# Performance work log

Hardware: AMD Instinct MI355X
Metric: run time of the kernel (lower is better)

Reference implementation:

```python
import jax, jax.numpy as jnp
import numpy as np

N0, K3, K2 = 262144, 27, 8
N1, N2 = N0 // 8, N0 // 64
CIN, C0, C1, C2 = 3, 24, 48, 96
EPS = 1e-5


def _conv_bn_relu(x, neigh, W, gamma, beta):
    # Octree sparse conv: gather neighbor features and contract with kernel.
    # x: [N, Cin], neigh: [M, K] int indices into N, W: [K, Cin, Cout]
    y = jnp.einsum('mkc,kcd->md', x[neigh], W)
    # BatchNorm1d (training-mode batch statistics) + ReLU
    mu = jnp.mean(y, axis=0)
    var = jnp.var(y, axis=0)
    y = (y - mu) * jax.lax.rsqrt(var + EPS) * gamma + beta
    return jax.nn.relu(y)


def setup_inputs() -> dict:
    key = jax.random.key(0)
    k = jax.random.split(key, 16)

    def w(kk, shape, fan):
        return jax.random.normal(kk, shape, jnp.float32) / np.float32(np.sqrt(fan))

    return {
        'data':   jax.random.normal(k[0], (N0, CIN), jnp.float32),
        'neigh0': jax.random.randint(k[1], (N0, K3), 0, N0, jnp.int32),
        'child0': jax.random.randint(k[2], (N1, K2), 0, N0, jnp.int32),
        'neigh1': jax.random.randint(k[3], (N1, K3), 0, N1, jnp.int32),
        'child1': jax.random.randint(k[4], (N2, K2), 0, N1, jnp.int32),
        'neigh2': jax.random.randint(k[5], (N2, K3), 0, N2, jnp.int32),
        'w0':  w(k[6],  (K3, CIN, C0), K3 * CIN),
        'g0':  jnp.ones((C0,), jnp.float32),  'b0':  jnp.zeros((C0,), jnp.float32),
        'wd0': w(k[7],  (K2, C0, C1),  K2 * C0),
        'gd0': jnp.ones((C1,), jnp.float32),  'bd0': jnp.zeros((C1,), jnp.float32),
        'w1':  w(k[8],  (K3, C1, C1),  K3 * C1),
        'g1':  jnp.ones((C1,), jnp.float32),  'b1':  jnp.zeros((C1,), jnp.float32),
        'wd1': w(k[9],  (K2, C1, C2),  K2 * C1),
        'gd1': jnp.ones((C2,), jnp.float32),  'bd1': jnp.zeros((C2,), jnp.float32),
        'wp':  w(k[10], (K3, C2, C2),  K3 * C2),
        'gp':  jnp.ones((C2,), jnp.float32),  'bp':  jnp.zeros((C2,), jnp.float32),
    }


def reference(data, neigh0, child0, neigh1, child1, neigh2,
              w0, g0, b0, wd0, gd0, bd0, w1, g1, b1, wd1, gd1, bd1, wp, gp, bp):
    # stage 0 at depth d: conv3 then stride-2 downsample
    x = _conv_bn_relu(data, neigh0, w0, g0, b0)      # [N0, 24]
    x = _conv_bn_relu(x, child0, wd0, gd0, bd0)      # [N1, 48]
    # stage 1 at depth d-1
    x = _conv_bn_relu(x, neigh1, w1, g1, b1)         # [N1, 48]
    x = _conv_bn_relu(x, child1, wd1, gd1, bd1)      # [N2, 96]
    # proj at depth d-2
    x = _conv_bn_relu(x, neigh2, wp, gp, bp)         # [N2, 96]
    return x
```

## Files before the change

kernel.cpp:

```cpp
#include <hip/hip_runtime.h>

#define N0 262144
#define N1 32768
#define N2 4096
#define EPSBN 1e-5f

typedef unsigned short ush_t;
typedef __bf16 bf16x8 __attribute__((ext_vector_type(8)));
typedef float  f32x4  __attribute__((ext_vector_type(4)));

union ufcast { unsigned int u; float f; };
__device__ __forceinline__ float bflo(unsigned int p) { ufcast x; x.u = p << 16;          return x.f; }
__device__ __forceinline__ float bfhi(unsigned int p) { ufcast x; x.u = p & 0xffff0000u; return x.f; }
__device__ __forceinline__ ush_t f2bf(float f) {
    ufcast x; x.f = f;
    unsigned int u = x.u + 0x7fffu + ((x.u >> 16) & 1u);
    return (ush_t)(u >> 16);
}
__device__ __forceinline__ bf16x8 as_bf8(uint4 u) {
    union { uint4 u; bf16x8 b; } x; x.u = u; return x.b;
}

template<int C, int NB>
__device__ __forceinline__ void compute_ss(const float* __restrict__ bins,
                                           const float* __restrict__ g, const float* __restrict__ b,
                                           float M, float* ssl)
{
    const int tid = threadIdx.x;
    if (tid < 2 * C) {
        float s = 0.f;
#pragma unroll
        for (int k = 0; k < NB; ++k) s += bins[k * 2 * C + tid];
        ssl[tid] = s;
    }
    __syncthreads();
    if (tid < C) {
        const float mu  = ssl[tid] / M;
        const float var = fmaxf(ssl[C + tid] / M - mu * mu, 0.f);
        const float sc  = g[tid] / sqrtf(var + EPSBN);
        const float sh  = b[tid] - mu * sc;
        ssl[tid] = sc; ssl[C + tid] = sh;
    }
    __syncthreads();
}

template<int K, int CIN, int CINP_W, int COUT, int COUTP, int NCH>
__device__ __forceinline__ void prep_stage(const float* __restrict__ W, ush_t* __restrict__ Wb, int e) {
    const int k  = e & 31;
    const int n  = (e >> 5) % COUTP;
    const int ch = e / (32 * COUTP);
    const int kp = ch * 32 + k;
    const int t  = kp / CINP_W;
    const int c  = kp % CINP_W;
    float v = 0.f;
    if (t < K && c < CIN && n < COUT) v = W[((size_t)t * CIN + c) * COUT + n];
    Wb[e] = f2bf(v);
}

#define BINS_TOTAL 9984

__global__ __launch_bounds__(256) void prep_all(
    const float* w0, const float* wd0, const float* w1, const float* wd1, const float* wp,
    const float* data,
    ush_t* wbA, ush_t* wbB, ush_t* wbC, ush_t* wbD, ush_t* wbE, ush_t* xa, float* binsz)
{
    const int e = blockIdx.x * 256 + threadIdx.x;
    switch (blockIdx.y) {
        case 0: if (e <   4096) prep_stage<27,  3,  4, 24, 32,  4>(w0,  wbA, e); break;
        case 1: if (e <  12288) prep_stage< 8, 24, 32, 48, 48,  8>(wd0, wbB, e); break;
        case 2: if (e <  64512) prep_stage<27, 48, 48, 48, 48, 42>(w1,  wbC, e); break;
        case 3: if (e <  49152) prep_stage< 8, 48, 64, 96, 96, 16>(wd1, wbD, e); break;
        case 4: if (e < 248832) prep_stage<27, 96, 96, 96, 96, 81>(wp,  wbE, e); break;
        case 5: if (e < N0) {
            const float* dp = data + (size_t)3 * e;
            unsigned int h0 = f2bf(dp[0]), h1 = f2bf(dp[1]), h2 = f2bf(dp[2]);
            uint2 v; v.x = h0 | (h1 << 16); v.y = h2;
            ((uint2*)xa)[e] = v;
        } break;
        case 6: if (e < BINS_TOTAL) binsz[e] = 0.f; break;
    }
}

__global__ __launch_bounds__(256) void mconvA_s(
    const ush_t* __restrict__ xa,
    const int*   __restrict__ neigh,
    const ush_t* __restrict__ Wb,
    ush_t*       __restrict__ y,
    float*       __restrict__ bins)
{
    __shared__ int   nl[3456];
    __shared__ float lsq[48];
    __shared__ ush_t ytile[128 * 24];
    const int tid = threadIdx.x;
    const int block0 = blockIdx.x * 128;

    {
        const uint4* src = (const uint4*)(neigh + (size_t)block0 * 27);
        uint4* dst = (uint4*)nl;
        for (int i = tid; i < 864; i += 256) dst[i] = src[i];
    }
    if (tid < 48) lsq[tid] = 0.f;
    __syncthreads();

    const int lane = tid & 63, wave = tid >> 6;
    const int quad = lane >> 4, l15 = lane & 15;

    f32x4 acc[2][2] = {};
#pragma unroll
    for (int g = 0; g < 2; ++g) {
        const int lr = g * 64 + wave * 16 + l15;
#pragma unroll
        for (int ch = 0; ch < 4; ++ch) {
            const int tA = ch * 8 + quad * 2;
            uint4 au = make_uint4(0, 0, 0, 0);
            if (ch < 3) {
                const uint2 lo = ((const uint2*)xa)[nl[lr * 27 + tA]];
                const uint2 hi = ((const uint2*)xa)[nl[lr * 27 + tA + 1]];
                au = make_uint4(lo.x, lo.y, hi.x, hi.y);
            } else {
                if (quad == 0) {
                    const uint2 lo = ((const uint2*)xa)[nl[lr * 27 + 24]];
                    const uint2 hi = ((const uint2*)xa)[nl[lr * 27 + 25]];
                    au = make_uint4(lo.x, lo.y, hi.x, hi.y);
                } else if (quad == 1) {
                    const uint2 lo = ((const uint2*)xa)[nl[lr * 27 + 26]];
                    au = make_uint4(lo.x, lo.y, 0, 0);
                }
            }
            const bf16x8 af = as_bf8(au);
#pragma unroll
            for (int ct = 0; ct < 2; ++ct) {
                const int n = ct * 16 + l15;
                const uint4 bu = *(const uint4*)(Wb + ((size_t)ch * 32 + n) * 32 + quad * 8);
                acc[g][ct] = __builtin_amdgcn_mfma_f32_16x16x32_bf16(af, as_bf8(bu), acc[g][ct], 0, 0, 0);
            }
        }
    }

#pragma unroll
    for (int g = 0; g < 2; ++g)
#pragma unroll
    for (int ct = 0; ct < 2; ++ct) {
        const int col = ct * 16 + l15;
        if (col < 24) {
            float s = 0.f, q = 0.f;
#pragma unroll
            for (int r = 0; r < 4; ++r) {
                const float v = acc[g][ct][r];
                ytile[(g * 64 + wave * 16 + quad * 4 + r) * 24 + col] = f2bf(v);
                s += v; q += v * v;
            }
            atomicAdd(&lsq[col], s);
            atomicAdd(&lsq[24 + col], q);
        }
    }
    __syncthreads();

    {
        const uint4* t4 = (const uint4*)ytile;
        uint4* dst = (uint4*)(y + (size_t)block0 * 24);
        for (int i = tid; i < 384; i += 256) dst[i] = t4[i];
    }
    if (tid < 48) atomicAdd(&bins[(blockIdx.x & 15) * 48 + tid], lsq[tid]);
}

__global__ __launch_bounds__(256) void mconvB_s(
    const ush_t* __restrict__ y0,
    const float* __restrict__ bins0,
    const float* __restrict__ g, const float* __restrict__ b,
    const int*   __restrict__ child,
    const ush_t* __restrict__ Wb,
    ush_t*       __restrict__ y1b,
    float*       __restrict__ bins1)
{
    __shared__ float ssl[48];
    __shared__ float lsq[96];
    __shared__ ush_t ytile[64 * 48];
    const int tid = threadIdx.x;
    if (tid < 96) lsq[tid] = 0.f;
    compute_ss<24, 16>(bins0, g, b, (float)N0, ssl);

    const int lane = tid & 63, wave = tid >> 6;
    const int quad = lane >> 4, l15 = lane & 15;
    const int rowA = blockIdx.x * 64 + wave * 16 + l15;
    const int c0 = quad * 8;

    float sc[8], sh[8];
    if (c0 < 24) {
#pragma unroll
        for (int j = 0; j < 8; ++j) { sc[j] = ssl[c0 + j]; sh[j] = ssl[24 + c0 + j]; }
    }

    const int4 c4a = *(const int4*)(child + (size_t)rowA * 8);
    const int4 c4b = *(const int4*)(child + (size_t)rowA * 8 + 4);
    const int idxs[8] = {c4a.x, c4a.y, c4a.z, c4a.w, c4b.x, c4b.y, c4b.z, c4b.w};

    f32x4 acc[3] = {};
#pragma unroll
    for (int ci = 0; ci < 8; ++ci) {
        const int idx = idxs[ci];
        uint4 au = make_uint4(0, 0, 0, 0);
        if (c0 < 24) {
            const uint4 raw = *(const uint4*)(y0 + (size_t)idx * 24 + c0);
            const unsigned int w4[4] = {raw.x, raw.y, raw.z, raw.w};
            unsigned int o4[4];
#pragma unroll
            for (int h = 0; h < 4; ++h) {
                const float a0 = fmaxf(bflo(w4[h]) * sc[2 * h]     + sh[2 * h],     0.f);
                const float a1 = fmaxf(bfhi(w4[h]) * sc[2 * h + 1] + sh[2 * h + 1], 0.f);
                o4[h] = (unsigned)f2bf(a0) | ((unsigned)f2bf(a1) << 16);
            }
            au = make_uint4(o4[0], o4[1], o4[2], o4[3]);
        }
        const bf16x8 af = as_bf8(au);
#pragma unroll
        for (int ct = 0; ct < 3; ++ct) {
            const int n = ct * 16 + l15;
            const uint4 bu = *(const uint4*)(Wb + ((size_t)ci * 48 + n) * 32 + quad * 8);
            acc[ct] = __builtin_amdgcn_mfma_f32_16x16x32_bf16(af, as_bf8(bu), acc[ct], 0, 0, 0);
        }
    }

#pragma unroll
    for (int ct = 0; ct < 3; ++ct) {
        const int col = ct * 16 + l15;
        float s = 0.f, q = 0.f;
#pragma unroll
        for (int r = 0; r < 4; ++r) {
            const float v = acc[ct][r];
            ytile[(wave * 16 + quad * 4 + r) * 48 + col] = f2bf(v);
            s += v; q += v * v;
        }
        atomicAdd(&lsq[col], s);
        atomicAdd(&lsq[48 + col], q);
    }
    __syncthreads();

    {
        const uint4* t4 = (const uint4*)ytile;
        uint4* dst = (uint4*)(y1b + (size_t)blockIdx.x * 64 * 48);
        for (int i = tid; i < 384; i += 256) dst[i] = t4[i];
    }
    if (tid < 96) atomicAdd(&bins1[(blockIdx.x & 15) * 96 + tid], lsq[tid]);
}

__global__ __launch_bounds__(256) void mconvC_s(
    const ush_t* __restrict__ y1b,
    const float* __restrict__ bins1,
    const float* __restrict__ g, const float* __restrict__ b,
    const int*   __restrict__ neigh,
    const ush_t* __restrict__ Wb,
    float*       __restrict__ y2,
    float*       __restrict__ bins2)
{
    __shared__ float ssl[96];
    __shared__ float lsq[96];
    __shared__ int   nl[1728];
    __shared__ float tile[64 * 48];
    const int tid = threadIdx.x;
    if (tid < 96) lsq[tid] = 0.f;

    {
        const uint4* src = (const uint4*)(neigh + (size_t)blockIdx.x * 1728);
        uint4* dst = (uint4*)nl;
        for (int i = tid; i < 432; i += 256) dst[i] = src[i];
    }
    compute_ss<48, 16>(bins1, g, b, (float)N1, ssl);

    const int lane = tid & 63, wave = tid >> 6;
    const int quad = lane >> 4, l15 = lane & 15;
    const int rl = wave * 16 + l15;

    int coffs[3], tofs[3];
    float sc[3][8], sh[3][8];
#pragma unroll
    for (int m3 = 0; m3 < 3; ++m3) {
        const int gg = 32 * m3 + 8 * quad;
        coffs[m3] = gg % 48;
        tofs[m3]  = gg / 48;
#pragma unroll
        for (int j = 0; j < 8; ++j) { sc[m3][j] = ssl[coffs[m3] + j]; sh[m3][j] = ssl[48 + coffs[m3] + j]; }
    }

    f32x4 acc[3] = {};
    for (int cg = 0; cg < 14; ++cg) {
#pragma unroll
        for (int m3 = 0; m3 < 3; ++m3) {
            const int ch = 3 * cg + m3;
            int t = 2 * cg + tofs[m3];
            if (t > 26) t = 26;
            const int idx = nl[rl * 27 + t];
            const uint4 raw = *(const uint4*)(y1b + (size_t)idx * 48 + coffs[m3]);
            const unsigned int w4[4] = {raw.x, raw.y, raw.z, raw.w};
            unsigned int o4[4];
#pragma unroll
            for (int h = 0; h < 4; ++h) {
                const float a0 = fmaxf(bflo(w4[h]) * sc[m3][2 * h]     + sh[m3][2 * h],     0.f);
                const float a1 = fmaxf(bfhi(w4[h]) * sc[m3][2 * h + 1] + sh[m3][2 * h + 1], 0.f);
                o4[h] = (unsigned)f2bf(a0) | ((unsigned)f2bf(a1) << 16);
            }
            const bf16x8 af = as_bf8(make_uint4(o4[0], o4[1], o4[2], o4[3]));
#pragma unroll
            for (int ct = 0; ct < 3; ++ct) {
                const int n = ct * 16 + l15;
                const uint4 bu = *(const uint4*)(Wb + ((size_t)ch * 48 + n) * 32 + quad * 8);
                acc[ct] = __builtin_amdgcn_mfma_f32_16x16x32_bf16(af, as_bf8(bu), acc[ct], 0, 0, 0);
            }
        }
    }

#pragma unroll
    for (int ct = 0; ct < 3; ++ct) {
        const int col = ct * 16 + l15;
        float s = 0.f, q = 0.f;
#pragma unroll
        for (int r = 0; r < 4; ++r) {
            const float v = acc[ct][r];
            tile[(wave * 16 + quad * 4 + r) * 48 + col] = v;
            s += v; q += v * v;
        }
        atomicAdd(&lsq[col], s);
        atomicAdd(&lsq[48 + col], q);
    }
    __syncthreads();

    {
        const uint4* t4 = (const uint4*)tile;
        uint4* dst = (uint4*)(y2 + (size_t)blockIdx.x * 64 * 48);
        for (int i = tid; i < 768; i += 256) dst[i] = t4[i];
    }
    if (tid < 96) atomicAdd(&bins2[(blockIdx.x & 15) * 96 + tid], lsq[tid]);
}

__global__ __launch_bounds__(256) void mconvD_s(
    const float* __restrict__ y2, const float* __restrict__ bins2,
    const float* __restrict__ g, const float* __restrict__ b,
    const int*   __restrict__ child,
    const ush_t* __restrict__ Wb,
    float*       __restrict__ y3,
    float*       __restrict__ bins3)
{
    __shared__ float ssl[96];
    __shared__ float tile[16 * 96];
    const int tid = threadIdx.x;
    for (int i = tid; i < 1536; i += 256) tile[i] = 0.f;
    compute_ss<48, 16>(bins2, g, b, (float)N1, ssl);

    const int lane = tid & 63, wave = tid >> 6;
    const int quad = lane >> 4, l15 = lane & 15;
    const int rowA = blockIdx.x * 16 + l15;

    const int2 c2 = *(const int2*)(child + (size_t)rowA * 8 + wave * 2);

    f32x4 acc[6] = {};
#pragma unroll
    for (int u = 0; u < 4; ++u) {
        const int ci = wave * 4 + u;
        const int sub = ci & 1;
        const int idx = (u >> 1) ? c2.y : c2.x;
        const int c0 = sub * 32 + quad * 8;
        uint4 au = make_uint4(0, 0, 0, 0);
        if (c0 < 48) {
            const float4 v0 = *(const float4*)(y2 + (size_t)idx * 48 + c0);
            const float4 v1 = *(const float4*)(y2 + (size_t)idx * 48 + c0 + 4);
            const float vv[8] = {v0.x, v0.y, v0.z, v0.w, v1.x, v1.y, v1.z, v1.w};
            unsigned int o4[4];
#pragma unroll
            for (int h = 0; h < 4; ++h) {
                const float a0 = fmaxf(vv[2 * h]     * ssl[c0 + 2 * h]     + ssl[48 + c0 + 2 * h],     0.f);
                const float a1 = fmaxf(vv[2 * h + 1] * ssl[c0 + 2 * h + 1] + ssl[48 + c0 + 2 * h + 1], 0.f);
                o4[h] = (unsigned)f2bf(a0) | ((unsigned)f2bf(a1) << 16);
            }
            au = make_uint4(o4[0], o4[1], o4[2], o4[3]);
        }
        const bf16x8 af = as_bf8(au);
#pragma unroll
        for (int ct = 0; ct < 6; ++ct) {
            const int n = ct * 16 + l15;
            const uint4 bu = *(const uint4*)(Wb + ((size_t)ci * 96 + n) * 32 + quad * 8);
            acc[ct] = __builtin_amdgcn_mfma_f32_16x16x32_bf16(af, as_bf8(bu), acc[ct], 0, 0, 0);
        }
    }

#pragma unroll
    for (int ct = 0; ct < 6; ++ct)
#pragma unroll
        for (int r = 0; r < 4; ++r)
            atomicAdd(&tile[(quad * 4 + r) * 96 + ct * 16 + l15], acc[ct][r]);
    __syncthreads();

    const size_t row0 = (size_t)blockIdx.x * 16;
    for (int i = tid; i < 1536; i += 256) y3[row0 * 96 + i] = tile[i];
    if (tid < 96) {
        float s = 0.f, q = 0.f;
#pragma unroll
        for (int r = 0; r < 16; ++r) { const float v = tile[r * 96 + tid]; s += v; q += v * v; }
        atomicAdd(&bins3[(blockIdx.x & 15) * 192 + tid], s);
        atomicAdd(&bins3[(blockIdx.x & 15) * 192 + 96 + tid], q);
    }
}

__global__ __launch_bounds__(256) void mconvE_s(
    const float* __restrict__ y3, const float* __restrict__ bins3,
    const float* __restrict__ g, const float* __restrict__ b,
    const int*   __restrict__ neigh,
    const ush_t* __restrict__ Wb,
    float*       __restrict__ y4,
    float*       __restrict__ bins4)
{
    __shared__ float ssl[192];
    __shared__ float tile[16 * 96];
    __shared__ int   nl[432];
    const int tid = threadIdx.x;
    for (int i = tid; i < 1536; i += 256) tile[i] = 0.f;

    {
        const uint4* src = (const uint4*)(neigh + (size_t)blockIdx.x * 432);
        uint4* dst = (uint4*)nl;
        for (int i = tid; i < 108; i += 256) dst[i] = src[i];
    }
    compute_ss<96, 16>(bins3, g, b, (float)N2, ssl);

    const int lane = tid & 63, wave = tid >> 6;
    const int quad = lane >> 4, l15 = lane & 15;

    const int ci0 = (wave == 0) ? 0 : 21 + (wave - 1) * 20;
    const int cnt = (wave == 0) ? 21 : 20;

    f32x4 acc[6] = {};
    for (int u = 0; u < cnt; ++u) {
        const int ci = ci0 + u;
        const int t = ci / 3, sub = ci % 3;
        const int idx = nl[l15 * 27 + t];
        const int c0 = sub * 32 + quad * 8;
        const float4 v0 = *(const float4*)(y3 + (size_t)idx * 96 + c0);
        const float4 v1 = *(const float4*)(y3 + (size_t)idx * 96 + c0 + 4);
        const float vv[8] = {v0.x, v0.y, v0.z, v0.w, v1.x, v1.y, v1.z, v1.w};
        unsigned int o4[4];
#pragma unroll
        for (int h = 0; h < 4; ++h) {
            const float a0 = fmaxf(vv[2 * h]     * ssl[c0 + 2 * h]     + ssl[96 + c0 + 2 * h],     0.f);
            const float a1 = fmaxf(vv[2 * h + 1] * ssl[c0 + 2 * h + 1] + ssl[96 + c0 + 2 * h + 1], 0.f);
            o4[h] = (unsigned)f2bf(a0) | ((unsigned)f2bf(a1) << 16);
        }
        const bf16x8 af = as_bf8(make_uint4(o4[0], o4[1], o4[2], o4[3]));
#pragma unroll
        for (int ct = 0; ct < 6; ++ct) {
            const int n = ct * 16 + l15;
            const uint4 bu = *(const uint4*)(Wb + ((size_t)ci * 96 + n) * 32 + quad * 8);
            acc[ct] = __builtin_amdgcn_mfma_f32_16x16x32_bf16(af, as_bf8(bu), acc[ct], 0, 0, 0);
        }
    }

#pragma unroll
    for (int ct = 0; ct < 6; ++ct)
#pragma unroll
        for (int r = 0; r < 4; ++r)
            atomicAdd(&tile[(quad * 4 + r) * 96 + ct * 16 + l15], acc[ct][r]);
    __syncthreads();

    const size_t row0 = (size_t)blockIdx.x * 16;
    for (int i = tid; i < 1536; i += 256) y4[row0 * 96 + i] = tile[i];
    if (tid < 96) {
        float s = 0.f, q = 0.f;
#pragma unroll
        for (int r = 0; r < 16; ++r) { const float v = tile[r * 96 + tid]; s += v; q += v * v; }
        atomicAdd(&bins4[(blockIdx.x & 15) * 192 + tid], s);
        atomicAdd(&bins4[(blockIdx.x & 15) * 192 + 96 + tid], q);
    }
}

__global__ __launch_bounds__(256) void writeout_s(
    const float* __restrict__ y4, const float* __restrict__ bins4,
    const float* __restrict__ g, const float* __restrict__ b,
    float* __restrict__ out)
{
    __shared__ float ssl[192];
    compute_ss<96, 16>(bins4, g, b, (float)N2, ssl);

    const int i = (blockIdx.x * 256 + threadIdx.x) * 4;
    const int c = i % 96;
    float4 v = *(const float4*)(y4 + i);
    float4 o;
    o.x = fmaxf(v.x * ssl[c + 0] + ssl[96 + c + 0], 0.f);
    o.y = fmaxf(v.y * ssl[c + 1] + ssl[96 + c + 1], 0.f);
    o.z = fmaxf(v.z * ssl[c + 2] + ssl[96 + c + 2], 0.f);
    o.w = fmaxf(v.w * ssl[c + 3] + ssl[96 + c + 3], 0.f);
    *(float4*)(out + i) = o;
}

extern "C" void kernel_launch(void* const* d_in, const int* in_sizes, int n_in,
                              void* d_out, int out_size, void* d_ws, size_t ws_size,
                              hipStream_t stream)
{
    const float* data   = (const float*)d_in[0];
    const int*   neigh0 = (const int*)d_in[1];
    const int*   child0 = (const int*)d_in[2];
    const int*   neigh1 = (const int*)d_in[3];
    const int*   child1 = (const int*)d_in[4];
    const int*   neigh2 = (const int*)d_in[5];
    const float* w0  = (const float*)d_in[6];
    const float* g0  = (const float*)d_in[7];
    const float* b0  = (const float*)d_in[8];
    const float* wd0 = (const float*)d_in[9];
    const float* gd0 = (const float*)d_in[10];
    const float* bd0 = (const float*)d_in[11];
    const float* w1  = (const float*)d_in[12];
    const float* g1  = (const float*)d_in[13];
    const float* b1  = (const float*)d_in[14];
    const float* wd1 = (const float*)d_in[15];
    const float* gd1 = (const float*)d_in[16];
    const float* bd1 = (const float*)d_in[17];
    const float* wp  = (const float*)d_in[18];
    const float* gp  = (const float*)d_in[19];
    const float* bp  = (const float*)d_in[20];
    float* out = (float*)d_out;

    float* wsf = (float*)d_ws;
    float* bins0 = wsf;
    float* bins1 = wsf + 768;
    float* bins2 = wsf + 2304;
    float* bins3 = wsf + 3840;
    float* bins4 = wsf + 6912;

    float* Y2  = wsf + 10240;
    float* Y3  = Y2 + (size_t)1572864;
    float* Y4  = Y3 + (size_t)393216;
    ush_t* Y0B = (ush_t*)(Y4 + (size_t)393216);
    ush_t* Y1B = Y0B + (size_t)6291456;
    ush_t* XA  = Y1B + (size_t)1572864;
    ush_t* WB  = XA + (size_t)1048576;

    ush_t* wbA = WB;
    ush_t* wbB = WB + 4096;
    ush_t* wbC = WB + 16384;
    ush_t* wbD = WB + 80896;
    ush_t* wbE = WB + 130048;

    prep_all<<<dim3(1024, 7), 256, 0, stream>>>(w0, wd0, w1, wd1, wp, data,
                                                wbA, wbB, wbC, wbD, wbE, XA, wsf);

    mconvA_s<<<N0 / 128, 256, 0, stream>>>(XA, neigh0, wbA, Y0B, bins0);
    mconvB_s<<<N1 / 64, 256, 0, stream>>>(Y0B, bins0, g0, b0, child0, wbB, Y1B, bins1);
    mconvC_s<<<N1 / 64, 256, 0, stream>>>(Y1B, bins1, gd0, bd0, neigh1, wbC, Y2, bins2);
    mconvD_s<<<N2 / 16, 256, 0, stream>>>(Y2, bins2, g1, b1, child1, wbD, Y3, bins3);
    mconvE_s<<<N2 / 16, 256, 0, stream>>>(Y3, bins3, gd1, bd1, neigh2, wbE, Y4, bins4);
    writeout_s<<<N2 * 96 / 4 / 256, 256, 0, stream>>>(Y4, bins4, gp, bp, out);

    (void)in_sizes; (void)n_in; (void)out_size; (void)ws_size;
}
```

Measured before the change: 236.6 us.

## Pre-normalize Y1 and Y3 into bf16 buffers before gather convolutions

Adds two elementwise kernels that apply BatchNorm scale/shift and ReLU once per element, writing bf16 copies of Y1 and Y3. The gather convolutions C and E then load these already-activated bf16 rows straight into MFMA operands, removing the per-gather normalization math that repeated up to 27 times per element. For E this also halves the bytes gathered (bf16 instead of fp32). The cost is two extra launches and an extra read/write pass over Y1 and Y3.

```diff
diff --git a/kernel.cpp b/kernel.cpp
--- a/kernel.cpp
+++ b/kernel.cpp
@@ -244,16 +244,37 @@
     if (tid < 96) atomicAdd(&bins1[(blockIdx.x & 15) * 96 + tid], lsq[tid]);
 }
 
+__global__ __launch_bounds__(256) void normY1(
+    const ush_t* __restrict__ y1b, const float* __restrict__ bins1,
+    const float* __restrict__ g, const float* __restrict__ b,
+    ush_t* __restrict__ y1n)
+{
+    __shared__ float ssl[96];
+    compute_ss<48, 16>(bins1, g, b, (float)N1, ssl);
+    const int tid = threadIdx.x;
+    const uint2* src = (const uint2*)y1b;
+    uint2* dst = (uint2*)y1n;
+#pragma unroll
+    for (int j = 0; j < 3; ++j) {
+        const int i = blockIdx.x * 768 + j * 256 + tid;
+        const uint2 p = src[i];
+        const int c = (4 * i) % 48;
+        uint2 o;
+        o.x = (unsigned)f2bf(fmaxf(bflo(p.x) * ssl[c + 0] + ssl[48 + c + 0], 0.f))
+            | ((unsigned)f2bf(fmaxf(bfhi(p.x) * ssl[c + 1] + ssl[48 + c + 1], 0.f)) << 16);
+        o.y = (unsigned)f2bf(fmaxf(bflo(p.y) * ssl[c + 2] + ssl[48 + c + 2], 0.f))
+            | ((unsigned)f2bf(fmaxf(bfhi(p.y) * ssl[c + 3] + ssl[48 + c + 3], 0.f)) << 16);
+        dst[i] = o;
+    }
+}
+
 __global__ __launch_bounds__(256) void mconvC_s(
-    const ush_t* __restrict__ y1b,
-    const float* __restrict__ bins1,
-    const float* __restrict__ g, const float* __restrict__ b,
+    const ush_t* __restrict__ y1n,
     const int*   __restrict__ neigh,
     const ush_t* __restrict__ Wb,
     float*       __restrict__ y2,
     float*       __restrict__ bins2)
 {
-    __shared__ float ssl[96];
     __shared__ float lsq[96];
     __shared__ int   nl[1728];
     __shared__ float tile[64 * 48];
@@ -265,21 +286,18 @@
         uint4* dst = (uint4*)nl;
         for (int i = tid; i < 432; i += 256) dst[i] = src[i];
     }
-    compute_ss<48, 16>(bins1, g, b, (float)N1, ssl);
+    __syncthreads();
 
     const int lane = tid & 63, wave = tid >> 6;
     const int quad = lane >> 4, l15 = lane & 15;
     const int rl = wave * 16 + l15;
 
     int coffs[3], tofs[3];
-    float sc[3][8], sh[3][8];
 #pragma unroll
     for (int m3 = 0; m3 < 3; ++m3) {
         const int gg = 32 * m3 + 8 * quad;
         coffs[m3] = gg % 48;
         tofs[m3]  = gg / 48;
-#pragma unroll
-        for (int j = 0; j < 8; ++j) { sc[m3][j] = ssl[coffs[m3] + j]; sh[m3][j] = ssl[48 + coffs[m3] + j]; }
     }
 
     f32x4 acc[3] = {};
@@ -290,16 +308,8 @@
             int t = 2 * cg + tofs[m3];
             if (t > 26) t = 26;
             const int idx = nl[rl * 27 + t];
-            const uint4 raw = *(const uint4*)(y1b + (size_t)idx * 48 + coffs[m3]);
-            const unsigned int w4[4] = {raw.x, raw.y, raw.z, raw.w};
-            unsigned int o4[4];
-#pragma unroll
-            for (int h = 0; h < 4; ++h) {
-                const float a0 = fmaxf(bflo(w4[h]) * sc[m3][2 * h]     + sh[m3][2 * h],     0.f);
-                const float a1 = fmaxf(bfhi(w4[h]) * sc[m3][2 * h + 1] + sh[m3][2 * h + 1], 0.f);
-                o4[h] = (unsigned)f2bf(a0) | ((unsigned)f2bf(a1) << 16);
-            }
-            const bf16x8 af = as_bf8(make_uint4(o4[0], o4[1], o4[2], o4[3]));
+            const uint4 raw = *(const uint4*)(y1n + (size_t)idx * 48 + coffs[m3]);
+            const bf16x8 af = as_bf8(raw);
 #pragma unroll
             for (int ct = 0; ct < 3; ++ct) {
                 const int n = ct * 16 + l15;
@@ -400,15 +410,32 @@
     }
 }
 
-__global__ __launch_bounds__(256) void mconvE_s(
+__global__ __launch_bounds__(256) void normY3(
     const float* __restrict__ y3, const float* __restrict__ bins3,
     const float* __restrict__ g, const float* __restrict__ b,
+    ush_t* __restrict__ y3n)
+{
+    __shared__ float ssl[192];
+    compute_ss<96, 16>(bins3, g, b, (float)N2, ssl);
+    const int tid = threadIdx.x;
+    uint* dst = (uint*)y3n;
+#pragma unroll
+    for (int j = 0; j < 3; ++j) {
+        const int i = blockIdx.x * 768 + j * 256 + tid;
+        const float2 p = ((const float2*)y3)[i];
+        const int c = (2 * i) % 96;
+        dst[i] = (unsigned)f2bf(fmaxf(p.x * ssl[c + 0] + ssl[96 + c + 0], 0.f))
+               | ((unsigned)f2bf(fmaxf(p.y * ssl[c + 1] + ssl[96 + c + 1], 0.f)) << 16);
+    }
+}
+
+__global__ __launch_bounds__(256) void mconvE_s(
+    const ush_t* __restrict__ y3n,
     const int*   __restrict__ neigh,
     const ush_t* __restrict__ Wb,
     float*       __restrict__ y4,
     float*       __restrict__ bins4)
 {
-    __shared__ float ssl[192];
     __shared__ float tile[16 * 96];
     __shared__ int   nl[432];
     const int tid = threadIdx.x;
@@ -419,7 +446,7 @@
         uint4* dst = (uint4*)nl;
         for (int i = tid; i < 108; i += 256) dst[i] = src[i];
     }
-    compute_ss<96, 16>(bins3, g, b, (float)N2, ssl);
+    __syncthreads();
 
     const int lane = tid & 63, wave = tid >> 6;
     const int quad = lane >> 4, l15 = lane & 15;
@@ -433,17 +460,8 @@
         const int t = ci / 3, sub = ci % 3;
         const int idx = nl[l15 * 27 + t];
         const int c0 = sub * 32 + quad * 8;
-        const float4 v0 = *(const float4*)(y3 + (size_t)idx * 96 + c0);
-        const float4 v1 = *(const float4*)(y3 + (size_t)idx * 96 + c0 + 4);
-        const float vv[8] = {v0.x, v0.y, v0.z, v0.w, v1.x, v1.y, v1.z, v1.w};
-        unsigned int o4[4];
-#pragma unroll
-        for (int h = 0; h < 4; ++h) {
-            const float a0 = fmaxf(vv[2 * h]     * ssl[c0 + 2 * h]     + ssl[96 + c0 + 2 * h],     0.f);
-            const float a1 = fmaxf(vv[2 * h + 1] * ssl[c0 + 2 * h + 1] + ssl[96 + c0 + 2 * h + 1], 0.f);
-            o4[h] = (unsigned)f2bf(a0) | ((unsigned)f2bf(a1) << 16);
-        }
-        const bf16x8 af = as_bf8(make_uint4(o4[0], o4[1], o4[2], o4[3]));
+        const uint4 raw = *(const uint4*)(y3n + (size_t)idx * 96 + c0);
+        const bf16x8 af = as_bf8(raw);
 #pragma unroll
         for (int ct = 0; ct < 6; ++ct) {
             const int n = ct * 16 + l15;
@@ -530,6 +548,8 @@
     ush_t* Y1B = Y0B + (size_t)6291456;
     ush_t* XA  = Y1B + (size_t)1572864;
     ush_t* WB  = XA + (size_t)1048576;
+    ush_t* Y1N = WB + (size_t)524288;
+    ush_t* Y3N = Y1N + (size_t)1572864;
 
     ush_t* wbA = WB;
     ush_t* wbB = WB + 4096;
@@ -542,9 +562,11 @@
 
     mconvA_s<<<N0 / 128, 256, 0, stream>>>(XA, neigh0, wbA, Y0B, bins0);
     mconvB_s<<<N1 / 64, 256, 0, stream>>>(Y0B, bins0, g0, b0, child0, wbB, Y1B, bins1);
-    mconvC_s<<<N1 / 64, 256, 0, stream>>>(Y1B, bins1, gd0, bd0, neigh1, wbC, Y2, bins2);
+    normY1<<<512, 256, 0, stream>>>(Y1B, bins1, gd0, bd0, Y1N);
+    mconvC_s<<<N1 / 64, 256, 0, stream>>>(Y1N, neigh1, wbC, Y2, bins2);
     mconvD_s<<<N2 / 16, 256, 0, stream>>>(Y2, bins2, g1, b1, child1, wbD, Y3, bins3);
-    mconvE_s<<<N2 / 16, 256, 0, stream>>>(Y3, bins3, gd1, bd1, neigh2, wbE, Y4, bins4);
+    normY3<<<256, 256, 0, stream>>>(Y3, bins3, gd1, bd1, Y3N);
+    mconvE_s<<<N2 / 16, 256, 0, stream>>>(Y3N, neigh2, wbE, Y4, bins4);
     writeout_s<<<N2 * 96 / 4 / 256, 256, 0, stream>>>(Y4, bins4, gp, bp, out);
 
     (void)in_sizes; (void)n_in; (void)out_size; (void)ws_size;
```

After: 244.3 us. 3.3% more time.

## Split K-reduction across two wave groups in mconvB and mconvC with LDS atomics

Applied to the files above, without the earlier changes.

mconvB and mconvC now launch 512 threads per block, and the two halves of the waves each handle half of the kernel taps (4 children or 7 channel groups) for the same 64 rows. Partial accumulators are combined with atomicAdd into a shared float tile. BN statistics are then computed by a serial column scan over that tile instead of per-wave atomics. The aim is more waves in flight to hide gather latency on these small grids (512 blocks), at the cost of LDS atomic traffic, an extra zeroing pass, and a slower serial 64-row stats loop.

```diff
diff --git a/kernel.cpp b/kernel.cpp
--- a/kernel.cpp
+++ b/kernel.cpp
@@ -164,7 +164,7 @@
     if (tid < 48) atomicAdd(&bins[(blockIdx.x & 15) * 48 + tid], lsq[tid]);
 }
 
-__global__ __launch_bounds__(256) void mconvB_s(
+__global__ __launch_bounds__(512) void mconvB_s(
     const ush_t* __restrict__ y0,
     const float* __restrict__ bins0,
     const float* __restrict__ g, const float* __restrict__ b,
@@ -174,15 +174,15 @@
     float*       __restrict__ bins1)
 {
     __shared__ float ssl[48];
-    __shared__ float lsq[96];
-    __shared__ ush_t ytile[64 * 48];
+    __shared__ float tile[3072];
     const int tid = threadIdx.x;
-    if (tid < 96) lsq[tid] = 0.f;
+    for (int i = tid; i < 3072; i += 512) tile[i] = 0.f;
     compute_ss<24, 16>(bins0, g, b, (float)N0, ssl);
 
     const int lane = tid & 63, wave = tid >> 6;
+    const int wgrp = wave & 3, half = wave >> 2;
     const int quad = lane >> 4, l15 = lane & 15;
-    const int rowA = blockIdx.x * 64 + wave * 16 + l15;
+    const int rowA = blockIdx.x * 64 + wgrp * 16 + l15;
     const int c0 = quad * 8;
 
     float sc[8], sh[8];
@@ -191,14 +191,14 @@
         for (int j = 0; j < 8; ++j) { sc[j] = ssl[c0 + j]; sh[j] = ssl[24 + c0 + j]; }
     }
 
-    const int4 c4a = *(const int4*)(child + (size_t)rowA * 8);
-    const int4 c4b = *(const int4*)(child + (size_t)rowA * 8 + 4);
-    const int idxs[8] = {c4a.x, c4a.y, c4a.z, c4a.w, c4b.x, c4b.y, c4b.z, c4b.w};
+    const int4 c4 = *(const int4*)(child + (size_t)rowA * 8 + half * 4);
+    const int idxs[4] = {c4.x, c4.y, c4.z, c4.w};
 
     f32x4 acc[3] = {};
 #pragma unroll
-    for (int ci = 0; ci < 8; ++ci) {
-        const int idx = idxs[ci];
+    for (int u = 0; u < 4; ++u) {
+        const int ci = half * 4 + u;
+        const int idx = idxs[u];
         uint4 au = make_uint4(0, 0, 0, 0);
         if (c0 < 24) {
             const uint4 raw = *(const uint4*)(y0 + (size_t)idx * 24 + c0);
@@ -222,29 +222,26 @@
     }
 
 #pragma unroll
-    for (int ct = 0; ct < 3; ++ct) {
-        const int col = ct * 16 + l15;
-        float s = 0.f, q = 0.f;
-#pragma unroll
-        for (int r = 0; r < 4; ++r) {
-            const float v = acc[ct][r];
-            ytile[(wave * 16 + quad * 4 + r) * 48 + col] = f2bf(v);
-            s += v; q += v * v;
-        }
-        atomicAdd(&lsq[col], s);
-        atomicAdd(&lsq[48 + col], q);
-    }
+    for (int ct = 0; ct < 3; ++ct)
+#pragma unroll
+        for (int r = 0; r < 4; ++r)
+            atomicAdd(&tile[(wgrp * 16 + quad * 4 + r) * 48 + ct * 16 + l15], acc[ct][r]);
     __syncthreads();
 
     {
-        const uint4* t4 = (const uint4*)ytile;
-        uint4* dst = (uint4*)(y1b + (size_t)blockIdx.x * 64 * 48);
-        for (int i = tid; i < 384; i += 256) dst[i] = t4[i];
-    }
-    if (tid < 96) atomicAdd(&bins1[(blockIdx.x & 15) * 96 + tid], lsq[tid]);
-}
-
-__global__ __launch_bounds__(256) void mconvC_s(
+        uint* dst = (uint*)(y1b + (size_t)blockIdx.x * 3072);
+        for (int i = tid; i < 1536; i += 512)
+            dst[i] = (unsigned)f2bf(tile[2 * i]) | ((unsigned)f2bf(tile[2 * i + 1]) << 16);
+    }
+    if (tid < 96) {
+        const int c = (tid < 48) ? tid : tid - 48;
+        float a = 0.f;
+        for (int r = 0; r < 64; ++r) { const float v = tile[r * 48 + c]; a += (tid < 48) ? v : v * v; }
+        atomicAdd(&bins1[(blockIdx.x & 15) * 96 + tid], a);
+    }
+}
+
+__global__ __launch_bounds__(512) void mconvC_s(
     const ush_t* __restrict__ y1b,
     const float* __restrict__ bins1,
     const float* __restrict__ g, const float* __restrict__ b,
@@ -254,22 +251,22 @@
     float*       __restrict__ bins2)
 {
     __shared__ float ssl[96];
-    __shared__ float lsq[96];
     __shared__ int   nl[1728];
-    __shared__ float tile[64 * 48];
+    __shared__ float tile[3072];
     const int tid = threadIdx.x;
-    if (tid < 96) lsq[tid] = 0.f;
+    for (int i = tid; i < 3072; i += 512) tile[i] = 0.f;
 
     {
         const uint4* src = (const uint4*)(neigh + (size_t)blockIdx.x * 1728);
         uint4* dst = (uint4*)nl;
-        for (int i = tid; i < 432; i += 256) dst[i] = src[i];
+        for (int i = tid; i < 432; i += 512) dst[i] = src[i];
     }
     compute_ss<48, 16>(bins1, g, b, (float)N1, ssl);
 
     const int lane = tid & 63, wave = tid >> 6;
+    const int wgrp = wave & 3, half = wave >> 2;
     const int quad = lane >> 4, l15 = lane & 15;
-    const int rl = wave * 16 + l15;
+    const int rl = wgrp * 16 + l15;
 
     int coffs[3], tofs[3];
     float sc[3][8], sh[3][8];
@@ -283,7 +280,8 @@
     }
 
     f32x4 acc[3] = {};
-    for (int cg = 0; cg < 14; ++cg) {
+    for (int cgi = 0; cgi < 7; ++cgi) {
+        const int cg = half * 7 + cgi;
 #pragma unroll
         for (int m3 = 0; m3 < 3; ++m3) {
             const int ch = 3 * cg + m3;
@@ -310,26 +308,23 @@
     }
 
 #pragma unroll
-    for (int ct = 0; ct < 3; ++ct) {
-        const int col = ct * 16 + l15;
-        float s = 0.f, q = 0.f;
-#pragma unroll
-        for (int r = 0; r < 4; ++r) {
-            const float v = acc[ct][r];
-            tile[(wave * 16 + quad * 4 + r) * 48 + col] = v;
-            s += v; q += v * v;
-        }
-        atomicAdd(&lsq[col], s);
-        atomicAdd(&lsq[48 + col], q);
-    }
+    for (int ct = 0; ct < 3; ++ct)
+#pragma unroll
+        for (int r = 0; r < 4; ++r)
+            atomicAdd(&tile[(wgrp * 16 + quad * 4 + r) * 48 + ct * 16 + l15], acc[ct][r]);
     __syncthreads();
 
     {
         const uint4* t4 = (const uint4*)tile;
-        uint4* dst = (uint4*)(y2 + (size_t)blockIdx.x * 64 * 48);
-        for (int i = tid; i < 768; i += 256) dst[i] = t4[i];
-    }
-    if (tid < 96) atomicAdd(&bins2[(blockIdx.x & 15) * 96 + tid], lsq[tid]);
+        uint4* dst = (uint4*)(y2 + (size_t)blockIdx.x * 3072);
+        for (int i = tid; i < 768; i += 512) dst[i] = t4[i];
+    }
+    if (tid < 96) {
+        const int c = (tid < 48) ? tid : tid - 48;
+        float a = 0.f;
+        for (int r = 0; r < 64; ++r) { const float v = tile[r * 48 + c]; a += (tid < 48) ? v : v * v; }
+        atomicAdd(&bins2[(blockIdx.x & 15) * 96 + tid], a);
+    }
 }
 
 __global__ __launch_bounds__(256) void mconvD_s(
@@ -541,8 +536,8 @@
                                                 wbA, wbB, wbC, wbD, wbE, XA, wsf);
 
     mconvA_s<<<N0 / 128, 256, 0, stream>>>(XA, neigh0, wbA, Y0B, bins0);
-    mconvB_s<<<N1 / 64, 256, 0, stream>>>(Y0B, bins0, g0, b0, child0, wbB, Y1B, bins1);
-    mconvC_s<<<N1 / 64, 256, 0, stream>>>(Y1B, bins1, gd0, bd0, neigh1, wbC, Y2, bins2);
+    mconvB_s<<<N1 / 64, 512, 0, stream>>>(Y0B, bins0, g0, b0, child0, wbB, Y1B, bins1);
+    mconvC_s<<<N1 / 64, 512, 0, stream>>>(Y1B, bins1, gd0, bd0, neigh1, wbC, Y2, bins2);
     mconvD_s<<<N2 / 16, 256, 0, stream>>>(Y2, bins2, g1, b1, child1, wbD, Y3, bins3);
     mconvE_s<<<N2 / 16, 256, 0, stream>>>(Y3, bins3, gd1, bd1, neigh2, wbE, Y4, bins4);
     writeout_s<<<N2 * 96 / 4 / 256, 256, 0, stream>>>(Y4, bins4, gp, bp, out);
```

Result: slower. 257.8 us (+9.0%).
